# Kernel tuning notes

Measured on AMD Instinct MI355X. Metric: run time of the kernel, lower is better.

Reference implementation:

```python
import jax, jax.numpy as jnp
import numpy as np

CNT_R = 500
DIM = 128
B, NEI = 8192, 64


def setup_inputs() -> dict:
    key = jax.random.key(0)
    ks = jax.random.split(key, 10)
    d2 = 2 * DIM
    return {
        "batch_nei_e_emb": jax.random.normal(ks[0], (B, NEI, DIM), dtype=jnp.float32),
        "batch_nei_rw": jax.random.uniform(ks[1], (B, NEI), dtype=jnp.float32),
        "w_r_table": jax.random.normal(ks[2], (2 * CNT_R + 1, DIM), dtype=jnp.float32),
        "zq_table": jax.random.normal(ks[3], (2 * CNT_R, DIM), dtype=jnp.float32),
        "attn_W_w": jax.random.normal(ks[4], (d2, d2), dtype=jnp.float32) / np.sqrt(d2),
        "attn_W_b": jnp.zeros((d2,), dtype=jnp.float32),
        "u_a_w": jax.random.normal(ks[5], (d2,), dtype=jnp.float32) / np.sqrt(d2),
        "u_a_b": jnp.zeros((), dtype=jnp.float32),
        "batch_nei_rid": jax.random.randint(ks[6], (B, NEI), 0, 2 * CNT_R + 1),
        "batch_q_rid": jax.random.randint(ks[7], (B,), 0, 2 * CNT_R),
    }


def reference(batch_nei_e_emb, batch_nei_rw, w_r_table, zq_table,
              attn_W_w, attn_W_b, u_a_w, u_a_b,
              batch_nei_rid, batch_q_rid):
    # gather relation hyperplane normals: (B, NEI, DIM)
    w_r = w_r_table[batch_nei_rid]
    n = w_r / jnp.linalg.norm(w_r, axis=-1, keepdims=True)
    # hyperplane projection: e - (e . n) n
    e = batch_nei_e_emb
    e_proj = e - jnp.sum(e * n, axis=-1, keepdims=True) * n
    # query relation embedding, tiled over neighbors: (B, NEI, DIM)
    z_q = zq_table[batch_q_rid]  # (B, DIM)
    z_q = jnp.broadcast_to(z_q[:, None, :], e_proj.shape)
    concat = jnp.concatenate([z_q, e_proj], axis=-1)  # (B, NEI, 2*DIM)
    h = jnp.tanh(jnp.einsum('bni,oi->bno', concat, attn_W_w) + attn_W_b)
    _alpha = jnp.einsum('bni,i->bn', h, u_a_w) + u_a_b  # (B, NEI)
    alpha = jax.nn.softmax(_alpha, axis=-1)
    attn = alpha + batch_nei_rw
    return attn
```

## Files before the change

kernel.cpp:

```cpp
#include <hip/hip_runtime.h>
#include <hip/hip_bf16.h>

#define NB    8192
#define NEI   64
#define DIM   128
#define D2    256
#define NR_W  1001
#define NR_Z  1000
#define EPB_LD 136
#define C2L2E 2.8853900817779268f

typedef __attribute__((ext_vector_type(8))) short bf16x8;
typedef __attribute__((ext_vector_type(4))) float f32x4;
typedef __attribute__((ext_vector_type(4))) unsigned int u32x4;

#define GLOAD16(dst, addr, OFF) \
    asm volatile("global_load_dwordx4 %0, %1, off offset:" OFF \
                 : "=v"(dst) : "v"(addr))

__device__ __forceinline__ ushort f2bf(float x) {
    union { float f; unsigned u; } c; c.f = x;
    unsigned u = c.u;
    return (ushort)((u + 0x7fffu + ((u >> 16) & 1u)) >> 16);
}

__device__ __forceinline__ unsigned pk2(float a, float b) {
    __hip_bfloat162 h = __float22bfloat162_rn(make_float2(a, b));
    return *(unsigned*)&h;
}

__device__ __forceinline__ bf16x8 asbf(u32x4 v) {
    union { u32x4 a; bf16x8 b; } u; u.a = v; return u.b;
}
__device__ __forceinline__ float4 asf4(u32x4 v) {
    union { u32x4 a; float4 b; } u; u.a = v; return u.b;
}


__global__ void k_norm(const float* __restrict__ w_r_table, float* __restrict__ norm_t) {
    int r = blockIdx.x;
    int t = threadIdx.x;
    float v = w_r_table[r * DIM + t];
    float s = v * v;
    #pragma unroll
    for (int m = 1; m < 64; m <<= 1) s += __shfl_xor(s, m);
    __shared__ float sh[2];
    if ((t & 63) == 0) sh[t >> 6] = s;
    __syncthreads();
    float tot = sh[0] + sh[1];
    norm_t[r * DIM + t] = v / sqrtf(tot);
}

__global__ void k_tq(const float* __restrict__ zq_table, const float* __restrict__ W,
                     const float* __restrict__ bias, float* __restrict__ tq_t) {
    int r = blockIdx.x;
    int o = threadIdx.x;
    __shared__ float4 z4[32];
    if (o < 32) z4[o] = ((const float4*)(zq_table + r * DIM))[o];
    __syncthreads();
    const float4* wr = (const float4*)(W + o * D2);
    float acc = bias[o];
    #pragma unroll 8
    for (int i = 0; i < 32; ++i) {
        float4 wv = wr[i], zv = z4[i];
        acc += wv.x*zv.x + wv.y*zv.y + wv.z*zv.z + wv.w*zv.w;
    }
    tq_t[r * D2 + o] = acc;
}

__global__ void k_bfrag(const float* __restrict__ W, ushort* __restrict__ bfrag) {
    int ot = blockIdx.x;
    int kt = blockIdx.y;
    int l  = threadIdx.x;
    int o  = ot * 16 + (l & 15);
    int k  = kt * 32 + (l >> 4) * 8;
    const float4* src = (const float4*)(W + o * D2 + DIM + k);
    float4 a = src[0], c = src[1];
    uint4 w;
    w.x = f2bf(a.x) | ((unsigned)f2bf(a.y) << 16);
    w.y = f2bf(a.z) | ((unsigned)f2bf(a.w) << 16);
    w.z = f2bf(c.x) | ((unsigned)f2bf(c.y) << 16);
    w.w = f2bf(c.z) | ((unsigned)f2bf(c.w) << 16);
    *(uint4*)(bfrag + ((ot * 4 + kt) * 64 + l) * 8) = w;
}

__global__ void k_sua(const float* __restrict__ u, float* __restrict__ sua) {
    int t = threadIdx.x;
    float v = u[t];
    #pragma unroll
    for (int m = 1; m < 64; m <<= 1) v += __shfl_xor(v, m);
    __shared__ float sh[4];
    if ((t & 63) == 0) sh[t >> 6] = v;
    __syncthreads();
    if (t == 0) sua[0] = sh[0] + sh[1] + sh[2] + sh[3];
}


__global__ __launch_bounds__(512, 2) void k_main(
    const float* __restrict__ e_emb,
    const float* __restrict__ rw,
    const int*   __restrict__ nei_rid,
    const int*   __restrict__ q_rid,
    const float* __restrict__ norm_t,
    const float* __restrict__ tq_t,
    const ushort* __restrict__ bfrag,
    const float* __restrict__ u_a_sum,
    const float* __restrict__ u_a_w,
    float* __restrict__ out)
{
    __shared__ __align__(16) ushort ep16[NEI * EPB_LD];
    __shared__ float alpw[8][NEI];

    const int t    = threadIdx.x;
    const int wave = t >> 6, lane = t & 63;
    const int ln   = lane & 15, hi = lane >> 4;
    const int rgrp = t >> 4, q4 = t & 15;
    const int b    = blockIdx.x;

    const char* bb0 = (const char*)bfrag + (((wave * 2) * 4 * 64) + lane) * 16;
    const char* bb1 = bb0 + 4096;
    u32x4 bq0, bq1, bq2, bq3, bq4, bq5, bq6, bq7;
    GLOAD16(bq0, bb0, "0");    GLOAD16(bq1, bb0, "1024");
    GLOAD16(bq2, bb0, "2048"); GLOAD16(bq3, bb0, "3072");
    GLOAD16(bq4, bb1, "0");    GLOAD16(bq5, bb1, "1024");
    GLOAD16(bq6, bb1, "2048"); GLOAD16(bq7, bb1, "3072");

    const int rid0 = nei_rid[b * NEI + rgrp];
    const int rid1 = nei_rid[b * NEI + 32 + rgrp];
    const char* ea = (const char*)(e_emb + ((size_t)b * NEI + rgrp) * DIM + q4 * 8);
    const char* eb = (const char*)(e_emb + ((size_t)b * NEI + 32 + rgrp) * DIM + q4 * 8);
    const char* na = (const char*)(norm_t + rid0 * DIM + q4 * 8);
    const char* nb = (const char*)(norm_t + rid1 * DIM + q4 * 8);
    u32x4 qea0, qea1, qeb0, qeb1, qna0, qna1, qnb0, qnb1;
    GLOAD16(qea0, ea, "0");  GLOAD16(qea1, ea, "16");
    GLOAD16(qeb0, eb, "0");  GLOAD16(qeb1, eb, "16");
    GLOAD16(qna0, na, "0");  GLOAD16(qna1, na, "16");
    GLOAD16(qnb0, nb, "0");  GLOAD16(qnb1, nb, "16");

    const int qr = q_rid[b];
    const float tq0 = tq_t[qr * D2 + wave * 32 + ln];
    const float tq1 = tq_t[qr * D2 + wave * 32 + 16 + ln];
    const float ua0 = u_a_w[wave * 32 + ln];
    const float ua1 = u_a_w[wave * 32 + 16 + ln];
    const float rwv = rw[(size_t)b * NEI + (t & 63)];
    const float sua = u_a_sum[0];

    asm volatile("s_waitcnt vmcnt(0)" ::: "memory");
    __builtin_amdgcn_sched_barrier(0);

    const float4 ea0 = asf4(qea0), ea1 = asf4(qea1);
    const float4 eb0 = asf4(qeb0), eb1 = asf4(qeb1);
    const float4 na0 = asf4(qna0), na1 = asf4(qna1);
    const float4 nb0 = asf4(qnb0), nb1 = asf4(qnb1);

    {
        float part = ea0.x*na0.x + ea0.y*na0.y + ea0.z*na0.z + ea0.w*na0.w
                   + ea1.x*na1.x + ea1.y*na1.y + ea1.z*na1.z + ea1.w*na1.w;
        part += __shfl_xor(part, 1);
        part += __shfl_xor(part, 2);
        part += __shfl_xor(part, 4);
        part += __shfl_xor(part, 8);
        const float d = part;
        float p0 = fmaf(-d, na0.x, ea0.x), p1 = fmaf(-d, na0.y, ea0.y);
        float p2 = fmaf(-d, na0.z, ea0.z), p3 = fmaf(-d, na0.w, ea0.w);
        float p4 = fmaf(-d, na1.x, ea1.x), p5 = fmaf(-d, na1.y, ea1.y);
        float p6 = fmaf(-d, na1.z, ea1.z), p7 = fmaf(-d, na1.w, ea1.w);
        uint4 w; w.x = pk2(p0,p1); w.y = pk2(p2,p3); w.z = pk2(p4,p5); w.w = pk2(p6,p7);
        *(uint4*)((char*)ep16 + rgrp * (EPB_LD*2) + q4 * 16) = w;
    }
    {
        float part = eb0.x*nb0.x + eb0.y*nb0.y + eb0.z*nb0.z + eb0.w*nb0.w
                   + eb1.x*nb1.x + eb1.y*nb1.y + eb1.z*nb1.z + eb1.w*nb1.w;
        part += __shfl_xor(part, 1);
        part += __shfl_xor(part, 2);
        part += __shfl_xor(part, 4);
        part += __shfl_xor(part, 8);
        const float d = part;
        float p0 = fmaf(-d, nb0.x, eb0.x), p1 = fmaf(-d, nb0.y, eb0.y);
        float p2 = fmaf(-d, nb0.z, eb0.z), p3 = fmaf(-d, nb0.w, eb0.w);
        float p4 = fmaf(-d, nb1.x, eb1.x), p5 = fmaf(-d, nb1.y, eb1.y);
        float p6 = fmaf(-d, nb1.z, eb1.z), p7 = fmaf(-d, nb1.w, eb1.w);
        uint4 w; w.x = pk2(p0,p1); w.y = pk2(p2,p3); w.z = pk2(p4,p5); w.w = pk2(p6,p7);
        *(uint4*)((char*)ep16 + (32 + rgrp) * (EPB_LD*2) + q4 * 16) = w;
    }

    __syncthreads();

    const bf16x8 bf00 = asbf(bq0), bf01 = asbf(bq1), bf02 = asbf(bq2), bf03 = asbf(bq3);
    const bf16x8 bf10 = asbf(bq4), bf11 = asbf(bq5), bf12 = asbf(bq6), bf13 = asbf(bq7);
    const float tqs0 = C2L2E * tq0, tqs1 = C2L2E * tq1;

    #pragma unroll
    for (int mt = 0; mt < 4; ++mt) {
        bf16x8 a_[4];
        #pragma unroll
        for (int kt = 0; kt < 4; ++kt)
            a_[kt] = *(const bf16x8*)&ep16[(mt*16 + ln) * EPB_LD + kt*32 + hi*8];
        f32x4 acc0 = (f32x4){0.f,0.f,0.f,0.f}, acc1 = (f32x4){0.f,0.f,0.f,0.f};
        acc0 = __builtin_amdgcn_mfma_f32_16x16x32_bf16(a_[0], bf00, acc0, 0, 0, 0);
        acc1 = __builtin_amdgcn_mfma_f32_16x16x32_bf16(a_[0], bf10, acc1, 0, 0, 0);
        acc0 = __builtin_amdgcn_mfma_f32_16x16x32_bf16(a_[1], bf01, acc0, 0, 0, 0);
        acc1 = __builtin_amdgcn_mfma_f32_16x16x32_bf16(a_[1], bf11, acc1, 0, 0, 0);
        acc0 = __builtin_amdgcn_mfma_f32_16x16x32_bf16(a_[2], bf02, acc0, 0, 0, 0);
        acc1 = __builtin_amdgcn_mfma_f32_16x16x32_bf16(a_[2], bf12, acc1, 0, 0, 0);
        acc0 = __builtin_amdgcn_mfma_f32_16x16x32_bf16(a_[3], bf03, acc0, 0, 0, 0);
        acc1 = __builtin_amdgcn_mfma_f32_16x16x32_bf16(a_[3], bf13, acc1, 0, 0, 0);
        float pr[4];
        #pragma unroll
        for (int j = 0; j < 4; ++j) {
            float ex0 = __builtin_exp2f(fmaf(C2L2E, acc0[j], tqs0));
            float ex1 = __builtin_exp2f(fmaf(C2L2E, acc1[j], tqs1));
            float r0  = __builtin_amdgcn_rcpf(ex0 + 1.f);
            float r1  = __builtin_amdgcn_rcpf(ex1 + 1.f);
            pr[j] = fmaf(ua0, r0, ua1 * r1);
        }
        #pragma unroll
        for (int m = 1; m < 16; m <<= 1)
            #pragma unroll
            for (int j = 0; j < 4; ++j) pr[j] += __shfl_xor(pr[j], m);
        if (ln == 0) {
            #pragma unroll
            for (int j = 0; j < 4; ++j) alpw[wave][mt*16 + hi*4 + j] = pr[j];
        }
    }

    __syncthreads();

    if (t < NEI) {
        float s8 = 0.f;
        #pragma unroll
        for (int w = 0; w < 8; ++w) s8 += alpw[w][t];
        float a = fmaf(-2.f, s8, sua);
        float p = __expf(a);
        float s = p;
        #pragma unroll
        for (int m = 1; m < 64; m <<= 1) s += __shfl_xor(s, m);
        out[(size_t)b * NEI + t] = fmaf(p, __builtin_amdgcn_rcpf(s), rwv);
    }
}


extern "C" void kernel_launch(void* const* d_in, const int* in_sizes, int n_in,
                              void* d_out, int out_size, void* d_ws, size_t ws_size,
                              hipStream_t stream) {
    const float* e_emb   = (const float*)d_in[0];
    const float* rw      = (const float*)d_in[1];
    const float* w_r_tab = (const float*)d_in[2];
    const float* zq_tab  = (const float*)d_in[3];
    const float* attn_W  = (const float*)d_in[4];
    const float* attn_b  = (const float*)d_in[5];
    const float* u_a_w   = (const float*)d_in[6];
    const int*   nei_rid = (const int*)d_in[8];
    const int*   q_rid   = (const int*)d_in[9];
    float* out = (float*)d_out;

    float* ws = (float*)d_ws;
    float* norm_t = ws;
    float* tq_t   = norm_t + NR_W * DIM;
    ushort* bfrag = (ushort*)(tq_t + NR_Z * D2);
    float* suap   = (float*)(bfrag + 16*4*64*8);

    k_norm<<<NR_W, DIM, 0, stream>>>(w_r_tab, norm_t);
    k_tq<<<NR_Z, D2, 0, stream>>>(zq_tab, attn_W, attn_b, tq_t);
    k_bfrag<<<dim3(16, 4), 64, 0, stream>>>(attn_W, bfrag);
    k_sua<<<1, 256, 0, stream>>>(u_a_w, suap);
    k_main<<<NB, 512, 0, stream>>>(e_emb, rw, nei_rid, q_rid,
                                   norm_t, tq_t, bfrag, suap, u_a_w, out);
}
```

Measured before the change: 135.8 us.

## Process four batch rows per block with software-prefetched next-row loads

Each block now handles four consecutive batch rows in a loop instead of one, so the per-block B-fragment weight loads and setup are amortized across rows. While the current row is projected and run through the MFMA attention, the embeddings, normals, query terms and rw values for the next row are issued as global loads, overlapping memory latency with compute. The grid shrinks by four, which lowers the number of resident blocks available to hide latency, and the prefetch buffers increase register pressure.

```diff
diff --git a/kernel.cpp b/kernel.cpp
--- a/kernel.cpp
+++ b/kernel.cpp
@@ -8,6 +8,7 @@
 #define NR_W  1001
 #define NR_Z  1000
 #define EPB_LD 136
+#define BPB   4
 #define C2L2E 2.8853900817779268f
 
 typedef __attribute__((ext_vector_type(8))) short bf16x8;
@@ -115,7 +116,7 @@
     const int wave = t >> 6, lane = t & 63;
     const int ln   = lane & 15, hi = lane >> 4;
     const int rgrp = t >> 4, q4 = t & 15;
-    const int b    = blockIdx.x;
+    const int b0   = blockIdx.x * BPB;
 
     const char* bb0 = (const char*)bfrag + (((wave * 2) * 4 * 64) + lane) * 16;
     const char* bb1 = bb0 + 4096;
@@ -125,117 +126,151 @@
     GLOAD16(bq4, bb1, "0");    GLOAD16(bq5, bb1, "1024");
     GLOAD16(bq6, bb1, "2048"); GLOAD16(bq7, bb1, "3072");
 
-    const int rid0 = nei_rid[b * NEI + rgrp];
-    const int rid1 = nei_rid[b * NEI + 32 + rgrp];
-    const char* ea = (const char*)(e_emb + ((size_t)b * NEI + rgrp) * DIM + q4 * 8);
-    const char* eb = (const char*)(e_emb + ((size_t)b * NEI + 32 + rgrp) * DIM + q4 * 8);
-    const char* na = (const char*)(norm_t + rid0 * DIM + q4 * 8);
-    const char* nb = (const char*)(norm_t + rid1 * DIM + q4 * 8);
-    u32x4 qea0, qea1, qeb0, qeb1, qna0, qna1, qnb0, qnb1;
-    GLOAD16(qea0, ea, "0");  GLOAD16(qea1, ea, "16");
-    GLOAD16(qeb0, eb, "0");  GLOAD16(qeb1, eb, "16");
-    GLOAD16(qna0, na, "0");  GLOAD16(qna1, na, "16");
-    GLOAD16(qnb0, nb, "0");  GLOAD16(qnb1, nb, "16");
-
-    const int qr = q_rid[b];
-    const float tq0 = tq_t[qr * D2 + wave * 32 + ln];
-    const float tq1 = tq_t[qr * D2 + wave * 32 + 16 + ln];
     const float ua0 = u_a_w[wave * 32 + ln];
     const float ua1 = u_a_w[wave * 32 + 16 + ln];
-    const float rwv = rw[(size_t)b * NEI + (t & 63)];
     const float sua = u_a_sum[0];
 
-    asm volatile("s_waitcnt vmcnt(0)" ::: "memory");
-    __builtin_amdgcn_sched_barrier(0);
-
-    const float4 ea0 = asf4(qea0), ea1 = asf4(qea1);
-    const float4 eb0 = asf4(qeb0), eb1 = asf4(qeb1);
-    const float4 na0 = asf4(qna0), na1 = asf4(qna1);
-    const float4 nb0 = asf4(qnb0), nb1 = asf4(qnb1);
-
+    int ridA = nei_rid[b0 * NEI + rgrp];
+    int ridB = nei_rid[b0 * NEI + 32 + rgrp];
+    u32x4 qea0, qea1, qeb0, qeb1, qna0, qna1, qnb0, qnb1;
     {
-        float part = ea0.x*na0.x + ea0.y*na0.y + ea0.z*na0.z + ea0.w*na0.w
-                   + ea1.x*na1.x + ea1.y*na1.y + ea1.z*na1.z + ea1.w*na1.w;
-        part += __shfl_xor(part, 1);
-        part += __shfl_xor(part, 2);
-        part += __shfl_xor(part, 4);
-        part += __shfl_xor(part, 8);
-        const float d = part;
-        float p0 = fmaf(-d, na0.x, ea0.x), p1 = fmaf(-d, na0.y, ea0.y);
-        float p2 = fmaf(-d, na0.z, ea0.z), p3 = fmaf(-d, na0.w, ea0.w);
-        float p4 = fmaf(-d, na1.x, ea1.x), p5 = fmaf(-d, na1.y, ea1.y);
-        float p6 = fmaf(-d, na1.z, ea1.z), p7 = fmaf(-d, na1.w, ea1.w);
-        uint4 w; w.x = pk2(p0,p1); w.y = pk2(p2,p3); w.z = pk2(p4,p5); w.w = pk2(p6,p7);
-        *(uint4*)((char*)ep16 + rgrp * (EPB_LD*2) + q4 * 16) = w;
-    }
+        const char* ea = (const char*)(e_emb + ((size_t)b0 * NEI + rgrp) * DIM + q4 * 8);
+        const char* eb = ea + 32 * DIM * 4;
+        GLOAD16(qea0, ea, "0");  GLOAD16(qea1, ea, "16");
+        GLOAD16(qeb0, eb, "0");  GLOAD16(qeb1, eb, "16");
+        const char* na = (const char*)(norm_t + ridA * DIM + q4 * 8);
+        const char* nb = (const char*)(norm_t + ridB * DIM + q4 * 8);
+        GLOAD16(qna0, na, "0");  GLOAD16(qna1, na, "16");
+        GLOAD16(qnb0, nb, "0");  GLOAD16(qnb1, nb, "16");
+    }
+    float tqp0, tqp1, rwp;
     {
-        float part = eb0.x*nb0.x + eb0.y*nb0.y + eb0.z*nb0.z + eb0.w*nb0.w
-                   + eb1.x*nb1.x + eb1.y*nb1.y + eb1.z*nb1.z + eb1.w*nb1.w;
-        part += __shfl_xor(part, 1);
-        part += __shfl_xor(part, 2);
-        part += __shfl_xor(part, 4);
-        part += __shfl_xor(part, 8);
-        const float d = part;
-        float p0 = fmaf(-d, nb0.x, eb0.x), p1 = fmaf(-d, nb0.y, eb0.y);
-        float p2 = fmaf(-d, nb0.z, eb0.z), p3 = fmaf(-d, nb0.w, eb0.w);
-        float p4 = fmaf(-d, nb1.x, eb1.x), p5 = fmaf(-d, nb1.y, eb1.y);
-        float p6 = fmaf(-d, nb1.z, eb1.z), p7 = fmaf(-d, nb1.w, eb1.w);
-        uint4 w; w.x = pk2(p0,p1); w.y = pk2(p2,p3); w.z = pk2(p4,p5); w.w = pk2(p6,p7);
-        *(uint4*)((char*)ep16 + (32 + rgrp) * (EPB_LD*2) + q4 * 16) = w;
-    }
-
-    __syncthreads();
-
-    const bf16x8 bf00 = asbf(bq0), bf01 = asbf(bq1), bf02 = asbf(bq2), bf03 = asbf(bq3);
-    const bf16x8 bf10 = asbf(bq4), bf11 = asbf(bq5), bf12 = asbf(bq6), bf13 = asbf(bq7);
-    const float tqs0 = C2L2E * tq0, tqs1 = C2L2E * tq1;
-
-    #pragma unroll
-    for (int mt = 0; mt < 4; ++mt) {
-        bf16x8 a_[4];
+        int qr = q_rid[b0];
+        tqp0 = tq_t[qr * D2 + wave * 32 + ln];
+        tqp1 = tq_t[qr * D2 + wave * 32 + 16 + ln];
+        rwp  = rw[(size_t)b0 * NEI + (t & 63)];
+    }
+    int ridAn = 0, ridBn = 0;
+    if (BPB > 1) {
+        ridAn = nei_rid[(b0 + 1) * NEI + rgrp];
+        ridBn = nei_rid[(b0 + 1) * NEI + 32 + rgrp];
+    }
+
+    #pragma unroll 1
+    for (int i = 0; i < BPB; ++i) {
+        const int b = b0 + i;
+
+        asm volatile("s_waitcnt vmcnt(0)" ::: "memory");
+        __builtin_amdgcn_sched_barrier(0);
+        const float4 ea0 = asf4(qea0), ea1 = asf4(qea1);
+        const float4 eb0 = asf4(qeb0), eb1 = asf4(qeb1);
+        const float4 na0 = asf4(qna0), na1 = asf4(qna1);
+        const float4 nb0 = asf4(qnb0), nb1 = asf4(qnb1);
+        const float tqs0 = C2L2E * tqp0, tqs1 = C2L2E * tqp1;
+        const float rwv  = rwp;
+
+        {
+            float part = ea0.x*na0.x + ea0.y*na0.y + ea0.z*na0.z + ea0.w*na0.w
+                       + ea1.x*na1.x + ea1.y*na1.y + ea1.z*na1.z + ea1.w*na1.w;
+            part += __shfl_xor(part, 1);
+            part += __shfl_xor(part, 2);
+            part += __shfl_xor(part, 4);
+            part += __shfl_xor(part, 8);
+            const float d = part;
+            float p0 = fmaf(-d, na0.x, ea0.x), p1 = fmaf(-d, na0.y, ea0.y);
+            float p2 = fmaf(-d, na0.z, ea0.z), p3 = fmaf(-d, na0.w, ea0.w);
+            float p4 = fmaf(-d, na1.x, ea1.x), p5 = fmaf(-d, na1.y, ea1.y);
+            float p6 = fmaf(-d, na1.z, ea1.z), p7 = fmaf(-d, na1.w, ea1.w);
+            uint4 w; w.x = pk2(p0,p1); w.y = pk2(p2,p3); w.z = pk2(p4,p5); w.w = pk2(p6,p7);
+            *(uint4*)((char*)ep16 + rgrp * (EPB_LD*2) + q4 * 16) = w;
+        }
+        {
+            float part = eb0.x*nb0.x + eb0.y*nb0.y + eb0.z*nb0.z + eb0.w*nb0.w
+                       + eb1.x*nb1.x + eb1.y*nb1.y + eb1.z*nb1.z + eb1.w*nb1.w;
+            part += __shfl_xor(part, 1);
+            part += __shfl_xor(part, 2);
+            part += __shfl_xor(part, 4);
+            part += __shfl_xor(part, 8);
+            const float d = part;
+            float p0 = fmaf(-d, nb0.x, eb0.x), p1 = fmaf(-d, nb0.y, eb0.y);
+            float p2 = fmaf(-d, nb0.z, eb0.z), p3 = fmaf(-d, nb0.w, eb0.w);
+            float p4 = fmaf(-d, nb1.x, eb1.x), p5 = fmaf(-d, nb1.y, eb1.y);
+            float p6 = fmaf(-d, nb1.z, eb1.z), p7 = fmaf(-d, nb1.w, eb1.w);
+            uint4 w; w.x = pk2(p0,p1); w.y = pk2(p2,p3); w.z = pk2(p4,p5); w.w = pk2(p6,p7);
+            *(uint4*)((char*)ep16 + (32 + rgrp) * (EPB_LD*2) + q4 * 16) = w;
+        }
+
+        if (i + 1 < BPB) {
+            const char* ea_n = (const char*)(e_emb + ((size_t)(b + 1) * NEI + rgrp) * DIM + q4 * 8);
+            const char* eb_n = ea_n + 32 * DIM * 4;
+            GLOAD16(qea0, ea_n, "0");  GLOAD16(qea1, ea_n, "16");
+            GLOAD16(qeb0, eb_n, "0");  GLOAD16(qeb1, eb_n, "16");
+            const char* na_n = (const char*)(norm_t + ridAn * DIM + q4 * 8);
+            const char* nb_n = (const char*)(norm_t + ridBn * DIM + q4 * 8);
+            GLOAD16(qna0, na_n, "0");  GLOAD16(qna1, na_n, "16");
+            GLOAD16(qnb0, nb_n, "0");  GLOAD16(qnb1, nb_n, "16");
+            int qr1 = q_rid[b + 1];
+            tqp0 = tq_t[qr1 * D2 + wave * 32 + ln];
+            tqp1 = tq_t[qr1 * D2 + wave * 32 + 16 + ln];
+            rwp  = rw[(size_t)(b + 1) * NEI + (t & 63)];
+            if (i + 2 < BPB) {
+                ridAn = nei_rid[(b + 2) * NEI + rgrp];
+                ridBn = nei_rid[(b + 2) * NEI + 32 + rgrp];
+            }
+        }
+
+        __syncthreads();
+
+        const bf16x8 bf00 = asbf(bq0), bf01 = asbf(bq1), bf02 = asbf(bq2), bf03 = asbf(bq3);
+        const bf16x8 bf10 = asbf(bq4), bf11 = asbf(bq5), bf12 = asbf(bq6), bf13 = asbf(bq7);
+
         #pragma unroll
-        for (int kt = 0; kt < 4; ++kt)
-            a_[kt] = *(const bf16x8*)&ep16[(mt*16 + ln) * EPB_LD + kt*32 + hi*8];
-        f32x4 acc0 = (f32x4){0.f,0.f,0.f,0.f}, acc1 = (f32x4){0.f,0.f,0.f,0.f};
-        acc0 = __builtin_amdgcn_mfma_f32_16x16x32_bf16(a_[0], bf00, acc0, 0, 0, 0);
-        acc1 = __builtin_amdgcn_mfma_f32_16x16x32_bf16(a_[0], bf10, acc1, 0, 0, 0);
-        acc0 = __builtin_amdgcn_mfma_f32_16x16x32_bf16(a_[1], bf01, acc0, 0, 0, 0);
-        acc1 = __builtin_amdgcn_mfma_f32_16x16x32_bf16(a_[1], bf11, acc1, 0, 0, 0);
-        acc0 = __builtin_amdgcn_mfma_f32_16x16x32_bf16(a_[2], bf02, acc0, 0, 0, 0);
-        acc1 = __builtin_amdgcn_mfma_f32_16x16x32_bf16(a_[2], bf12, acc1, 0, 0, 0);
-        acc0 = __builtin_amdgcn_mfma_f32_16x16x32_bf16(a_[3], bf03, acc0, 0, 0, 0);
-        acc1 = __builtin_amdgcn_mfma_f32_16x16x32_bf16(a_[3], bf13, acc1, 0, 0, 0);
-        float pr[4];
-        #pragma unroll
-        for (int j = 0; j < 4; ++j) {
-            float ex0 = __builtin_exp2f(fmaf(C2L2E, acc0[j], tqs0));
-            float ex1 = __builtin_exp2f(fmaf(C2L2E, acc1[j], tqs1));
-            float r0  = __builtin_amdgcn_rcpf(ex0 + 1.f);
-            float r1  = __builtin_amdgcn_rcpf(ex1 + 1.f);
-            pr[j] = fmaf(ua0, r0, ua1 * r1);
-        }
-        #pragma unroll
-        for (int m = 1; m < 16; m <<= 1)
-            #pragma unroll
-            for (int j = 0; j < 4; ++j) pr[j] += __shfl_xor(pr[j], m);
-        if (ln == 0) {
-            #pragma unroll
-            for (int j = 0; j < 4; ++j) alpw[wave][mt*16 + hi*4 + j] = pr[j];
-        }
-    }
-
-    __syncthreads();
-
-    if (t < NEI) {
-        float s8 = 0.f;
-        #pragma unroll
-        for (int w = 0; w < 8; ++w) s8 += alpw[w][t];
-        float a = fmaf(-2.f, s8, sua);
-        float p = __expf(a);
-        float s = p;
-        #pragma unroll
-        for (int m = 1; m < 64; m <<= 1) s += __shfl_xor(s, m);
-        out[(size_t)b * NEI + t] = fmaf(p, __builtin_amdgcn_rcpf(s), rwv);
+        for (int mt = 0; mt < 4; ++mt) {
+            bf16x8 a_[4];
+            #pragma unroll
+            for (int kt = 0; kt < 4; ++kt)
+                a_[kt] = *(const bf16x8*)&ep16[(mt*16 + ln) * EPB_LD + kt*32 + hi*8];
+            f32x4 acc0 = (f32x4){0.f,0.f,0.f,0.f}, acc1 = (f32x4){0.f,0.f,0.f,0.f};
+            acc0 = __builtin_amdgcn_mfma_f32_16x16x32_bf16(a_[0], bf00, acc0, 0, 0, 0);
+            acc1 = __builtin_amdgcn_mfma_f32_16x16x32_bf16(a_[0], bf10, acc1, 0, 0, 0);
+            acc0 = __builtin_amdgcn_mfma_f32_16x16x32_bf16(a_[1], bf01, acc0, 0, 0, 0);
+            acc1 = __builtin_amdgcn_mfma_f32_16x16x32_bf16(a_[1], bf11, acc1, 0, 0, 0);
+            acc0 = __builtin_amdgcn_mfma_f32_16x16x32_bf16(a_[2], bf02, acc0, 0, 0, 0);
+            acc1 = __builtin_amdgcn_mfma_f32_16x16x32_bf16(a_[2], bf12, acc1, 0, 0, 0);
+            acc0 = __builtin_amdgcn_mfma_f32_16x16x32_bf16(a_[3], bf03, acc0, 0, 0, 0);
+            acc1 = __builtin_amdgcn_mfma_f32_16x16x32_bf16(a_[3], bf13, acc1, 0, 0, 0);
+            float pr[4];
+            #pragma unroll
+            for (int j = 0; j < 4; ++j) {
+                float ex0 = __builtin_exp2f(fmaf(C2L2E, acc0[j], tqs0));
+                float ex1 = __builtin_exp2f(fmaf(C2L2E, acc1[j], tqs1));
+                float r0  = __builtin_amdgcn_rcpf(ex0 + 1.f);
+                float r1  = __builtin_amdgcn_rcpf(ex1 + 1.f);
+                pr[j] = fmaf(ua0, r0, ua1 * r1);
+            }
+            #pragma unroll
+            for (int m = 1; m < 16; m <<= 1)
+                #pragma unroll
+                for (int j = 0; j < 4; ++j) pr[j] += __shfl_xor(pr[j], m);
+            if (ln == 0) {
+                #pragma unroll
+                for (int j = 0; j < 4; ++j) alpw[wave][mt*16 + hi*4 + j] = pr[j];
+            }
+        }
+
+        __syncthreads();
+
+        if (t < NEI) {
+            float s8 = 0.f;
+            #pragma unroll
+            for (int w = 0; w < 8; ++w) s8 += alpw[w][t];
+            float a = fmaf(-2.f, s8, sua);
+            float p = __expf(a);
+            float s = p;
+            #pragma unroll
+            for (int m = 1; m < 64; m <<= 1) s += __shfl_xor(s, m);
+            out[(size_t)b * NEI + t] = fmaf(p, __builtin_amdgcn_rcpf(s), rwv);
+        }
     }
 }
 
@@ -264,6 +299,6 @@
     k_tq<<<NR_Z, D2, 0, stream>>>(zq_tab, attn_W, attn_b, tq_t);
     k_bfrag<<<dim3(16, 4), 64, 0, stream>>>(attn_W, bfrag);
     k_sua<<<1, 256, 0, stream>>>(u_a_w, suap);
-    k_main<<<NB, 512, 0, stream>>>(e_emb, rw, nei_rid, q_rid,
-                                   norm_t, tq_t, bfrag, suap, u_a_w, out);
-}
+    k_main<<<NB / BPB, 512, 0, stream>>>(e_emb, rw, nei_rid, q_rid,
+                                         norm_t, tq_t, bfrag, suap, u_a_w, out);
+}
```

After: 137.7 us. About the same (+1.4%).

## Process eight batches per block with async global-to-LDS prefetch of embeddings

Applied to the files above, without the earlier changes.

The main kernel now handles eight batch rows per block in a loop. The next row's 32 KB embedding tile is prefetched into a swizzled LDS buffer with global_load_lds while the current row runs its MFMA and softmax work, and the norm vectors, tq values and rw are prefetched into registers. A new per-batch k_tqd kernel materializes the scaled query-bias rows so the main loop avoids an indirect lookup, at the cost of an extra 8 MB write and read. The intent is to hide global-load latency and amortize the bfrag loads across rows. The trade-offs are a large LDS footprint that lowers occupancy and only 1024 blocks in the grid.

```diff
diff --git a/kernel.cpp b/kernel.cpp
--- a/kernel.cpp
+++ b/kernel.cpp
@@ -8,6 +8,7 @@
 #define NR_W  1001
 #define NR_Z  1000
 #define EPB_LD 136
+#define BPB   8
 #define C2L2E 2.8853900817779268f
 
 typedef __attribute__((ext_vector_type(8))) short bf16x8;
@@ -32,8 +33,11 @@
 __device__ __forceinline__ bf16x8 asbf(u32x4 v) {
     union { u32x4 a; bf16x8 b; } u; u.a = v; return u.b;
 }
-__device__ __forceinline__ float4 asf4(u32x4 v) {
-    union { u32x4 a; float4 b; } u; u.a = v; return u.b;
+
+__device__ __forceinline__ void gll16(const void* g, void* l) {
+    __builtin_amdgcn_global_load_lds(
+        (const __attribute__((address_space(1))) unsigned int*)g,
+        (__attribute__((address_space(3))) unsigned int*)l, 16, 0, 0);
 }
 
 
@@ -68,6 +72,13 @@
     tq_t[r * D2 + o] = acc;
 }
 
+__global__ void k_tqd(const float* __restrict__ tq_t, const int* __restrict__ q_rid,
+                      float* __restrict__ tqd) {
+    int b = blockIdx.x;
+    int o = threadIdx.x;
+    tqd[(size_t)b * D2 + o] = C2L2E * tq_t[q_rid[b] * D2 + o];
+}
+
 __global__ void k_bfrag(const float* __restrict__ W, ushort* __restrict__ bfrag) {
     int ot = blockIdx.x;
     int kt = blockIdx.y;
@@ -100,22 +111,22 @@
     const float* __restrict__ e_emb,
     const float* __restrict__ rw,
     const int*   __restrict__ nei_rid,
-    const int*   __restrict__ q_rid,
     const float* __restrict__ norm_t,
-    const float* __restrict__ tq_t,
+    const float* __restrict__ tqd,
     const ushort* __restrict__ bfrag,
     const float* __restrict__ u_a_sum,
     const float* __restrict__ u_a_w,
     float* __restrict__ out)
 {
+    __shared__ __align__(16) float  e_raw[NEI * DIM];
     __shared__ __align__(16) ushort ep16[NEI * EPB_LD];
     __shared__ float alpw[8][NEI];
 
     const int t    = threadIdx.x;
     const int wave = t >> 6, lane = t & 63;
     const int ln   = lane & 15, hi = lane >> 4;
-    const int rgrp = t >> 4, q4 = t & 15;
-    const int b    = blockIdx.x;
+    const int row  = t >> 3, q3 = t & 7;
+    const int b0   = blockIdx.x * BPB;
 
     const char* bb0 = (const char*)bfrag + (((wave * 2) * 4 * 64) + lane) * 16;
     const char* bb1 = bb0 + 4096;
@@ -125,117 +136,143 @@
     GLOAD16(bq4, bb1, "0");    GLOAD16(bq5, bb1, "1024");
     GLOAD16(bq6, bb1, "2048"); GLOAD16(bq7, bb1, "3072");
 
-    const int rid0 = nei_rid[b * NEI + rgrp];
-    const int rid1 = nei_rid[b * NEI + 32 + rgrp];
-    const char* ea = (const char*)(e_emb + ((size_t)b * NEI + rgrp) * DIM + q4 * 8);
-    const char* eb = (const char*)(e_emb + ((size_t)b * NEI + 32 + rgrp) * DIM + q4 * 8);
-    const char* na = (const char*)(norm_t + rid0 * DIM + q4 * 8);
-    const char* nb = (const char*)(norm_t + rid1 * DIM + q4 * 8);
-    u32x4 qea0, qea1, qeb0, qeb1, qna0, qna1, qnb0, qnb1;
-    GLOAD16(qea0, ea, "0");  GLOAD16(qea1, ea, "16");
-    GLOAD16(qeb0, eb, "0");  GLOAD16(qeb1, eb, "16");
-    GLOAD16(qna0, na, "0");  GLOAD16(qna1, na, "16");
-    GLOAD16(qnb0, nb, "0");  GLOAD16(qnb1, nb, "16");
-
-    const int qr = q_rid[b];
-    const float tq0 = tq_t[qr * D2 + wave * 32 + ln];
-    const float tq1 = tq_t[qr * D2 + wave * 32 + 16 + ln];
     const float ua0 = u_a_w[wave * 32 + ln];
     const float ua1 = u_a_w[wave * 32 + 16 + ln];
-    const float rwv = rw[(size_t)b * NEI + (t & 63)];
     const float sua = u_a_sum[0];
 
-    asm volatile("s_waitcnt vmcnt(0)" ::: "memory");
-    __builtin_amdgcn_sched_barrier(0);
-
-    const float4 ea0 = asf4(qea0), ea1 = asf4(qea1);
-    const float4 eb0 = asf4(qeb0), eb1 = asf4(qeb1);
-    const float4 na0 = asf4(qna0), na1 = asf4(qna1);
-    const float4 nb0 = asf4(qnb0), nb1 = asf4(qnb1);
-
+    unsigned soff[4];
+    #pragma unroll
+    for (int c = 0; c < 4; ++c) {
+        unsigned D = (unsigned)(wave*4096 + c*1024 + lane*16);
+        unsigned r7 = (D >> 9) & 7;
+        soff[c] = D ^ (r7 << 4);
+    }
+    const char* ebase = (const char*)e_emb;
+
+    int ridn;
+    float4 nv0, nv1, nv2, nv3;
     {
-        float part = ea0.x*na0.x + ea0.y*na0.y + ea0.z*na0.z + ea0.w*na0.w
-                   + ea1.x*na1.x + ea1.y*na1.y + ea1.z*na1.z + ea1.w*na1.w;
-        part += __shfl_xor(part, 1);
-        part += __shfl_xor(part, 2);
-        part += __shfl_xor(part, 4);
-        part += __shfl_xor(part, 8);
-        const float d = part;
-        float p0 = fmaf(-d, na0.x, ea0.x), p1 = fmaf(-d, na0.y, ea0.y);
-        float p2 = fmaf(-d, na0.z, ea0.z), p3 = fmaf(-d, na0.w, ea0.w);
-        float p4 = fmaf(-d, na1.x, ea1.x), p5 = fmaf(-d, na1.y, ea1.y);
-        float p6 = fmaf(-d, na1.z, ea1.z), p7 = fmaf(-d, na1.w, ea1.w);
-        uint4 w; w.x = pk2(p0,p1); w.y = pk2(p2,p3); w.z = pk2(p4,p5); w.w = pk2(p6,p7);
-        *(uint4*)((char*)ep16 + rgrp * (EPB_LD*2) + q4 * 16) = w;
+        int ridc = nei_rid[b0 * NEI + row];
+        const float4* np = (const float4*)(norm_t + ridc * DIM + q3 * 16);
+        nv0 = np[0]; nv1 = np[1]; nv2 = np[2]; nv3 = np[3];
+        ridn = (BPB > 1) ? nei_rid[(b0 + 1) * NEI + row] : 0;
     }
-    {
-        float part = eb0.x*nb0.x + eb0.y*nb0.y + eb0.z*nb0.z + eb0.w*nb0.w
-                   + eb1.x*nb1.x + eb1.y*nb1.y + eb1.z*nb1.z + eb1.w*nb1.w;
-        part += __shfl_xor(part, 1);
-        part += __shfl_xor(part, 2);
-        part += __shfl_xor(part, 4);
-        part += __shfl_xor(part, 8);
-        const float d = part;
-        float p0 = fmaf(-d, nb0.x, eb0.x), p1 = fmaf(-d, nb0.y, eb0.y);
-        float p2 = fmaf(-d, nb0.z, eb0.z), p3 = fmaf(-d, nb0.w, eb0.w);
-        float p4 = fmaf(-d, nb1.x, eb1.x), p5 = fmaf(-d, nb1.y, eb1.y);
-        float p6 = fmaf(-d, nb1.z, eb1.z), p7 = fmaf(-d, nb1.w, eb1.w);
-        uint4 w; w.x = pk2(p0,p1); w.y = pk2(p2,p3); w.z = pk2(p4,p5); w.w = pk2(p6,p7);
-        *(uint4*)((char*)ep16 + (32 + rgrp) * (EPB_LD*2) + q4 * 16) = w;
-    }
-
-    __syncthreads();
-
-    const bf16x8 bf00 = asbf(bq0), bf01 = asbf(bq1), bf02 = asbf(bq2), bf03 = asbf(bq3);
-    const bf16x8 bf10 = asbf(bq4), bf11 = asbf(bq5), bf12 = asbf(bq6), bf13 = asbf(bq7);
-    const float tqs0 = C2L2E * tq0, tqs1 = C2L2E * tq1;
-
+    float tqc0 = tqd[(size_t)b0 * D2 + wave * 32 + ln];
+    float tqc1 = tqd[(size_t)b0 * D2 + wave * 32 + 16 + ln];
+    float rwc  = rw[(size_t)b0 * NEI + (t & 63)];
+    float tqn0 = 0.f, tqn1 = 0.f, rwn = 0.f;
     #pragma unroll
-    for (int mt = 0; mt < 4; ++mt) {
-        bf16x8 a_[4];
+    for (int c = 0; c < 4; ++c)
+        gll16(ebase + (((size_t)b0) << 15) + soff[c], (char*)e_raw + wave*4096 + c*1024);
+
+    #pragma unroll 1
+    for (int i = 0; i < BPB; ++i) {
+        const int b = b0 + i;
+
+        asm volatile("s_waitcnt vmcnt(0)" ::: "memory");
+        __builtin_amdgcn_sched_barrier(0);
+        __builtin_amdgcn_s_barrier();
+        __builtin_amdgcn_sched_barrier(0);
+
+        {
+            const unsigned rbase = (unsigned)(row * 512 + q3 * 64);
+            const unsigned rx = (unsigned)((row & 7) << 4);
+            float4 e0 = *(const float4*)((const char*)e_raw + ((rbase +  0) ^ rx));
+            float4 e1 = *(const float4*)((const char*)e_raw + ((rbase + 16) ^ rx));
+            float4 e2 = *(const float4*)((const char*)e_raw + ((rbase + 32) ^ rx));
+            float4 e3 = *(const float4*)((const char*)e_raw + ((rbase + 48) ^ rx));
+            float part = e0.x*nv0.x + e0.y*nv0.y + e0.z*nv0.z + e0.w*nv0.w
+                       + e1.x*nv1.x + e1.y*nv1.y + e1.z*nv1.z + e1.w*nv1.w
+                       + e2.x*nv2.x + e2.y*nv2.y + e2.z*nv2.z + e2.w*nv2.w
+                       + e3.x*nv3.x + e3.y*nv3.y + e3.z*nv3.z + e3.w*nv3.w;
+            part += __shfl_xor(part, 1);
+            part += __shfl_xor(part, 2);
+            part += __shfl_xor(part, 4);
+            const float d = part;
+            float p0 = fmaf(-d, nv0.x, e0.x), p1 = fmaf(-d, nv0.y, e0.y);
+            float p2 = fmaf(-d, nv0.z, e0.z), p3 = fmaf(-d, nv0.w, e0.w);
+            float p4 = fmaf(-d, nv1.x, e1.x), p5 = fmaf(-d, nv1.y, e1.y);
+            float p6 = fmaf(-d, nv1.z, e1.z), p7 = fmaf(-d, nv1.w, e1.w);
+            uint4 w0; w0.x = pk2(p0,p1); w0.y = pk2(p2,p3); w0.z = pk2(p4,p5); w0.w = pk2(p6,p7);
+            float s0 = fmaf(-d, nv2.x, e2.x), s1 = fmaf(-d, nv2.y, e2.y);
+            float s2 = fmaf(-d, nv2.z, e2.z), s3 = fmaf(-d, nv2.w, e2.w);
+            float s4 = fmaf(-d, nv3.x, e3.x), s5 = fmaf(-d, nv3.y, e3.y);
+            float s6 = fmaf(-d, nv3.z, e3.z), s7 = fmaf(-d, nv3.w, e3.w);
+            uint4 w1; w1.x = pk2(s0,s1); w1.y = pk2(s2,s3); w1.z = pk2(s4,s5); w1.w = pk2(s6,s7);
+            char* dst = (char*)ep16 + row * (EPB_LD*2) + q3 * 32;
+            *(uint4*)dst = w0;
+            *(uint4*)(dst + 16) = w1;
+        }
+
+        asm volatile("s_waitcnt lgkmcnt(0)" ::: "memory");
+        __builtin_amdgcn_s_barrier();
+        __builtin_amdgcn_sched_barrier(0);
+
+        if (i + 1 < BPB) {
+            const float4* np = (const float4*)(norm_t + ridn * DIM + q3 * 16);
+            nv0 = np[0]; nv1 = np[1]; nv2 = np[2]; nv3 = np[3];
+            if (i + 2 < BPB) ridn = nei_rid[(b + 2) * NEI + row];
+            tqn0 = tqd[(size_t)(b + 1) * D2 + wave * 32 + ln];
+            tqn1 = tqd[(size_t)(b + 1) * D2 + wave * 32 + 16 + ln];
+            rwn  = rw[(size_t)(b + 1) * NEI + (t & 63)];
+            #pragma unroll
+            for (int c = 0; c < 4; ++c)
+                gll16(ebase + (((size_t)(b + 1)) << 15) + soff[c],
+                      (char*)e_raw + wave*4096 + c*1024);
+        }
+        __builtin_amdgcn_sched_barrier(0);
+
         #pragma unroll
-        for (int kt = 0; kt < 4; ++kt)
-            a_[kt] = *(const bf16x8*)&ep16[(mt*16 + ln) * EPB_LD + kt*32 + hi*8];
-        f32x4 acc0 = (f32x4){0.f,0.f,0.f,0.f}, acc1 = (f32x4){0.f,0.f,0.f,0.f};
-        acc0 = __builtin_amdgcn_mfma_f32_16x16x32_bf16(a_[0], bf00, acc0, 0, 0, 0);
-        acc1 = __builtin_amdgcn_mfma_f32_16x16x32_bf16(a_[0], bf10, acc1, 0, 0, 0);
-        acc0 = __builtin_amdgcn_mfma_f32_16x16x32_bf16(a_[1], bf01, acc0, 0, 0, 0);
-        acc1 = __builtin_amdgcn_mfma_f32_16x16x32_bf16(a_[1], bf11, acc1, 0, 0, 0);
-        acc0 = __builtin_amdgcn_mfma_f32_16x16x32_bf16(a_[2], bf02, acc0, 0, 0, 0);
-        acc1 = __builtin_amdgcn_mfma_f32_16x16x32_bf16(a_[2], bf12, acc1, 0, 0, 0);
-        acc0 = __builtin_amdgcn_mfma_f32_16x16x32_bf16(a_[3], bf03, acc0, 0, 0, 0);
-        acc1 = __builtin_amdgcn_mfma_f32_16x16x32_bf16(a_[3], bf13, acc1, 0, 0, 0);
-        float pr[4];
-        #pragma unroll
-        for (int j = 0; j < 4; ++j) {
-            float ex0 = __builtin_exp2f(fmaf(C2L2E, acc0[j], tqs0));
-            float ex1 = __builtin_exp2f(fmaf(C2L2E, acc1[j], tqs1));
-            float r0  = __builtin_amdgcn_rcpf(ex0 + 1.f);
-            float r1  = __builtin_amdgcn_rcpf(ex1 + 1.f);
-            pr[j] = fmaf(ua0, r0, ua1 * r1);
+        for (int mt = 0; mt < 4; ++mt) {
+            bf16x8 a_[4];
+            #pragma unroll
+            for (int kt = 0; kt < 4; ++kt)
+                a_[kt] = *(const bf16x8*)&ep16[(mt*16 + ln) * EPB_LD + kt*32 + hi*8];
+            f32x4 acc0 = (f32x4){0.f,0.f,0.f,0.f}, acc1 = (f32x4){0.f,0.f,0.f,0.f};
+            acc0 = __builtin_amdgcn_mfma_f32_16x16x32_bf16(a_[0], asbf(bq0), acc0, 0, 0, 0);
+            acc1 = __builtin_amdgcn_mfma_f32_16x16x32_bf16(a_[0], asbf(bq4), acc1, 0, 0, 0);
+            acc0 = __builtin_amdgcn_mfma_f32_16x16x32_bf16(a_[1], asbf(bq1), acc0, 0, 0, 0);
+            acc1 = __builtin_amdgcn_mfma_f32_16x16x32_bf16(a_[1], asbf(bq5), acc1, 0, 0, 0);
+            acc0 = __builtin_amdgcn_mfma_f32_16x16x32_bf16(a_[2], asbf(bq2), acc0, 0, 0, 0);
+            acc1 = __builtin_amdgcn_mfma_f32_16x16x32_bf16(a_[2], asbf(bq6), acc1, 0, 0, 0);
+            acc0 = __builtin_amdgcn_mfma_f32_16x16x32_bf16(a_[3], asbf(bq3), acc0, 0, 0, 0);
+            acc1 = __builtin_amdgcn_mfma_f32_16x16x32_bf16(a_[3], asbf(bq7), acc1, 0, 0, 0);
+            float pr[4];
+            #pragma unroll
+            for (int j = 0; j < 4; ++j) {
+                float ex0 = __builtin_exp2f(fmaf(C2L2E, acc0[j], tqc0));
+                float ex1 = __builtin_exp2f(fmaf(C2L2E, acc1[j], tqc1));
+                float r0  = __builtin_amdgcn_rcpf(ex0 + 1.f);
+                float r1  = __builtin_amdgcn_rcpf(ex1 + 1.f);
+                pr[j] = fmaf(ua0, r0, ua1 * r1);
+            }
+            #pragma unroll
+            for (int m = 1; m < 16; m <<= 1)
+                #pragma unroll
+                for (int j = 0; j < 4; ++j) pr[j] += __shfl_xor(pr[j], m);
+            if (ln == 0) {
+                #pragma unroll
+                for (int j = 0; j < 4; ++j) alpw[wave][mt*16 + hi*4 + j] = pr[j];
+            }
         }
-        #pragma unroll
-        for (int m = 1; m < 16; m <<= 1)
-            #pragma unroll
-            for (int j = 0; j < 4; ++j) pr[j] += __shfl_xor(pr[j], m);
-        if (ln == 0) {
-            #pragma unroll
-            for (int j = 0; j < 4; ++j) alpw[wave][mt*16 + hi*4 + j] = pr[j];
+
+        asm volatile("s_waitcnt lgkmcnt(0)" ::: "memory");
+        __builtin_amdgcn_s_barrier();
+        __builtin_amdgcn_sched_barrier(0);
+
+        if (t < NEI) {
+            float s8 = 0.f;
+            #pragma unroll
+            for (int w = 0; w < 8; ++w) s8 += alpw[w][t];
+            float a = fmaf(-2.f, s8, sua);
+            float p = __expf(a);
+            float s = p;
+            #pragma unroll
+            for (int m = 1; m < 64; m <<= 1) s += __shfl_xor(s, m);
+            out[(size_t)b * NEI + t] = fmaf(p, __builtin_amdgcn_rcpf(s), rwc);
         }
-    }
-
-    __syncthreads();
-
-    if (t < NEI) {
-        float s8 = 0.f;
-        #pragma unroll
-        for (int w = 0; w < 8; ++w) s8 += alpw[w][t];
-        float a = fmaf(-2.f, s8, sua);
-        float p = __expf(a);
-        float s = p;
-        #pragma unroll
-        for (int m = 1; m < 64; m <<= 1) s += __shfl_xor(s, m);
-        out[(size_t)b * NEI + t] = fmaf(p, __builtin_amdgcn_rcpf(s), rwv);
+
+        if (i + 1 < BPB) { tqc0 = tqn0; tqc1 = tqn1; rwc = rwn; }
     }
 }
 
@@ -259,11 +296,13 @@
     float* tq_t   = norm_t + NR_W * DIM;
     ushort* bfrag = (ushort*)(tq_t + NR_Z * D2);
     float* suap   = (float*)(bfrag + 16*4*64*8);
+    float* tqd    = suap + 4;
 
     k_norm<<<NR_W, DIM, 0, stream>>>(w_r_tab, norm_t);
     k_tq<<<NR_Z, D2, 0, stream>>>(zq_tab, attn_W, attn_b, tq_t);
+    k_tqd<<<NB, D2, 0, stream>>>(tq_t, q_rid, tqd);
     k_bfrag<<<dim3(16, 4), 64, 0, stream>>>(attn_W, bfrag);
     k_sua<<<1, 256, 0, stream>>>(u_a_w, suap);
-    k_main<<<NB, 512, 0, stream>>>(e_emb, rw, nei_rid, q_rid,
-                                   norm_t, tq_t, bfrag, suap, u_a_w, out);
-}
+    k_main<<<NB / BPB, 512, 0, stream>>>(e_emb, rw, nei_rid,
+                                         norm_t, tqd, bfrag, suap, u_a_w, out);
+}
```

After: 181.8 us. +33.9%, slower.
